# Kernel optimization log

Hardware: AMD Instinct MI355X
Metric: run time of the kernel (lower is better)

The kernel has to match this reference:

```python
import jax, jax.numpy as jnp
import numpy as np
import math

T = 1024      # num tokens
D = 1024      # hidden_size
H = 16        # attention heads
KV = 4        # kv heads
DH = 64       # head_dim
E = 8         # routed experts
K = 2         # top-k
F = 512       # moe_intermediate_size
FS = 2048     # shared_expert_intermediate_size
L = 2         # layers
V = 4096      # codec vocab
THETA = 1e6
EPS = 1e-6


def rms(x, w):
    return x * jax.lax.rsqrt(jnp.mean(x * x, -1, keepdims=True) + EPS) * w


def rope(x, pos):
    # x: [T, h, DH], rotate-half (non-interleaved) rotary
    half = DH // 2
    inv = 1.0 / (THETA ** (jnp.arange(half, dtype=jnp.float32) / half))
    ang = pos.astype(jnp.float32)[:, None] * inv          # [T, half]
    cos = jnp.concatenate([jnp.cos(ang)] * 2, -1)[:, None, :]
    sin = jnp.concatenate([jnp.sin(ang)] * 2, -1)[:, None, :]
    rot = jnp.concatenate([-x[..., half:], x[..., :half]], -1)
    return x * cos + rot * sin


def setup_inputs() -> dict:
    key = jax.random.key(0)
    ks = jax.random.split(key, 20)
    s = 0.02
    n = lambda k, shp: jax.random.normal(k, shp, dtype=jnp.float32) * s
    return {
        "input_ids": jax.random.randint(ks[0], (T,), 0, V),
        "positions": jnp.arange(T),
        "emb": n(ks[1], (V, D)),
        "ln1": jnp.ones((L, D), jnp.float32),
        "wq": n(ks[2], (L, D, H * DH)),
        "wk": n(ks[3], (L, D, KV * DH)),
        "wv": n(ks[4], (L, D, KV * DH)),
        "wo": n(ks[5], (L, H * DH, D)),
        "qn": jnp.ones((L, DH), jnp.float32),
        "kn": jnp.ones((L, DH), jnp.float32),
        "ln2": jnp.ones((L, D), jnp.float32),
        "router_w": n(ks[6], (L, D, E)),
        "egu": n(ks[7], (L, E, D, 2 * F)),
        "edn": n(ks[8], (L, E, F, D)),
        "sgu": n(ks[9], (L, D, 2 * FS)),
        "sdn": n(ks[10], (L, FS, D)),
        "sg_gate": n(ks[11], (L, D)),
        "final_ln": jnp.ones((D,), jnp.float32),
    }


def forward(input_ids, positions, emb, ln1, wq, wk, wv, wo, qn, kn, ln2,
            router_w, egu, edn, sgu, sdn, sg_gate, final_ln):
    h = emb[input_ids]                          # [T, D]
    res = jnp.zeros_like(h)
    causal = jnp.tril(jnp.ones((T, T), bool))
    scale = 1.0 / math.sqrt(DH)
    for i in range(L):
        # --- attention (pre-norm, fused add-residual semantics) ---
        res = h + res
        hn = rms(res, ln1[i])
        q = rms((hn @ wq[i]).reshape(T, H, DH), qn[i])
        k = rms((hn @ wk[i]).reshape(T, KV, DH), kn[i])
        v = (hn @ wv[i]).reshape(T, KV, DH)
        q, k = rope(q, positions), rope(k, positions)
        k = jnp.repeat(k, H // KV, axis=1)      # GQA expand
        v = jnp.repeat(v, H // KV, axis=1)
        att = jnp.einsum('qhd,khd->hqk', q, k) * scale
        att = jnp.where(causal[None], att, -jnp.inf)
        att = jax.nn.softmax(att, axis=-1)
        o = jnp.einsum('hqk,khd->qhd', att, v).reshape(T, H * DH) @ wo[i]
        # --- MoE MLP with shared expert ---
        res = o + res
        hn = rms(res, ln2[i])
        # shared expert: SiluAndMul + down, gated by sigmoid scalar
        gu = hn @ sgu[i]
        shared = (jax.nn.silu(gu[:, :FS]) * gu[:, FS:]) @ sdn[i]
        shared = shared * jax.nn.sigmoid(hn @ sg_gate[i])[:, None]
        # routed experts: softmax router, top-k, renormalize
        probs = jax.nn.softmax(hn @ router_w[i], axis=-1)      # [T, E]
        w, idx = jax.lax.top_k(probs, K)
        w = w / jnp.sum(w, -1, keepdims=True)
        comb = jnp.zeros((T, E), hn.dtype).at[jnp.arange(T)[:, None], idx].add(w)
        g = jnp.einsum('td,edf->tef', hn, egu[i])              # [T, E, 2F]
        he = jax.nn.silu(g[..., :F]) * g[..., F:]              # [T, E, F]
        routed = jnp.einsum('tef,efd,te->td', he, edn[i], comb)
        h = routed + shared
    res = h + res
    return rms(res, final_ln)


def reference(input_ids, positions, emb, ln1, wq, wk, wv, wo, qn, kn, ln2,
              router_w, egu, edn, sgu, sdn, sg_gate, final_ln):
    return forward(input_ids, positions, emb, ln1, wq, wk, wv, wo, qn, kn, ln2,
                   router_w, egu, edn, sgu, sdn, sg_gate, final_ln)
```

## Files before the change

kernel.cpp:

```cpp
#include <hip/hip_runtime.h>
#include <hip/hip_bf16.h>

#define T_ 1024
#define D_ 1024
#define H_ 16
#define KV_ 4
#define DH_ 64
#define E_ 8
#define TOPK_ 2
#define F_ 512
#define FS_ 2048
#define L_ 2

typedef unsigned int uint32;
typedef __attribute__((ext_vector_type(8))) short short8;
typedef __attribute__((ext_vector_type(4))) short short4v;
typedef __attribute__((ext_vector_type(4))) float f32x4;

__device__ __forceinline__ short f2bf(float f){
  uint32 u = __float_as_uint(f);
  return (short)((u + 0x7fffu + ((u >> 16) & 1u)) >> 16);
}
__device__ __forceinline__ float bf2f(short s){
  return __uint_as_float(((uint32)(unsigned short)s) << 16);
}

__device__ __forceinline__ void split8(const float* src, short8& h8, short8& l8){
  #pragma unroll
  for (int j = 0; j < 8; j++){
    short hi = f2bf(src[j]);
    h8[j] = hi;
    l8[j] = f2bf(src[j] - bf2f(hi));
  }
}

__global__ void k_embed(const int* __restrict__ ids, const float* __restrict__ emb,
                        float* __restrict__ h, float* __restrict__ res){
  int idx = blockIdx.x * 256 + threadIdx.x;
  int t = idx >> 10, d = idx & 1023;
  h[idx] = emb[(size_t)ids[t] * D_ + d];
  res[idx] = 0.f;
}

__global__ void k_zero_i32(int* __restrict__ p, int n){
  int i = blockIdx.x * 64 + threadIdx.x;
  if (i < n) p[i] = 0;
}

__global__ __launch_bounds__(256)
void k_fused_rms(float* __restrict__ res, const float* __restrict__ h,
                 const float* __restrict__ w, float* __restrict__ out){
  int t = blockIdx.x, tid = threadIdx.x;
  float* rr = res + (size_t)t * D_;
  const float* hr = h + (size_t)t * D_;
  float ss = 0.f;
  float vloc[4];
  #pragma unroll
  for (int u = 0; u < 4; u++){
    int d = tid + u * 256;
    float v = rr[d] + hr[d];
    vloc[u] = v;
    ss += v * v;
  }
  #pragma unroll
  for (int o = 32; o; o >>= 1) ss += __shfl_xor(ss, o);
  __shared__ float red[4];
  if ((tid & 63) == 0) red[tid >> 6] = ss;
  __syncthreads();
  float r = rsqrtf((red[0] + red[1] + red[2] + red[3]) * (1.f / D_) + 1e-6f);
  float* orow = out + (size_t)t * D_;
  #pragma unroll
  for (int u = 0; u < 4; u++){
    int d = tid + u * 256;
    rr[d] = vloc[u];
    orow[d] = vloc[u] * r * w[d];
  }
}

__global__ __launch_bounds__(256)
void k_fused_rms2(float* __restrict__ res, const float* __restrict__ h0,
                  const float* __restrict__ h1,
                  const float* __restrict__ w, float* __restrict__ out){
  int t = blockIdx.x, tid = threadIdx.x;
  float* rr = res + (size_t)t * D_;
  const float* h0r = h0 + (size_t)t * D_;
  const float* h1r = h1 + (size_t)t * D_;
  float ss = 0.f;
  float vloc[4];
  #pragma unroll
  for (int u = 0; u < 4; u++){
    int d = tid + u * 256;
    float v = rr[d] + h0r[d] + h1r[d];
    vloc[u] = v;
    ss += v * v;
  }
  #pragma unroll
  for (int o = 32; o; o >>= 1) ss += __shfl_xor(ss, o);
  __shared__ float red[4];
  if ((tid & 63) == 0) red[tid >> 6] = ss;
  __syncthreads();
  float r = rsqrtf((red[0] + red[1] + red[2] + red[3]) * (1.f / D_) + 1e-6f);
  float* orow = out + (size_t)t * D_;
  #pragma unroll
  for (int u = 0; u < 4; u++){
    int d = tid + u * 256;
    rr[d] = vloc[u];
    orow[d] = vloc[u] * r * w[d];
  }
}

__global__ __launch_bounds__(64)
void k_qknorm_rope(float* __restrict__ buf, const float* __restrict__ nw,
                   const int* __restrict__ pos, int nheads){
  int row = blockIdx.x;
  int t = row / nheads;
  int lane = threadIdx.x;
  int base = row * DH_ + lane;
  float x = buf[base];
  float ss = x * x;
  #pragma unroll
  for (int o = 32; o; o >>= 1) ss += __shfl_xor(ss, o);
  float r = rsqrtf(ss * (1.f / DH_) + 1e-6f);
  float xn = x * r * nw[lane];
  int j = lane & 31;
  float inv = powf(1.0e6f, -(float)j * (1.f / 32.f));
  float ang = (float)pos[t] * inv;
  float s, c;
  sincosf(ang, &s, &c);
  float p = __shfl_xor(xn, 32);
  float rot = (lane < 32) ? -p : p;
  buf[base] = xn * c + rot * s;
}

__global__ __launch_bounds__(256)
void k_fattn(const float* __restrict__ q, const float* __restrict__ k,
             const float* __restrict__ v, float* __restrict__ out){
  const int h = blockIdx.x, qt = blockIdx.y;
  const int kvh = h >> 2;
  const int tid = threadIdx.x;
  const int w = tid >> 6, lane = tid & 63, l16 = lane & 15, lq = lane >> 4;

  __shared__ __align__(16) short Kh[64][72], Kl[64][72];
  __shared__ __align__(16) short Vth[64][72], Vtl[64][72];
  __shared__ __align__(16) short Ph[64][72], Pl[64][72];

  short8 qh[2], ql[2];
  {
    const float* qp = q + ((size_t)(qt * 64 + w * 16 + l16) * H_ + h) * DH_;
    #pragma unroll
    for (int s = 0; s < 2; s++){
      float a8[8];
      *(float4*)&a8[0] = *(const float4*)(qp + lq * 8 + 32 * s);
      *(float4*)&a8[4] = *(const float4*)(qp + lq * 8 + 32 * s + 4);
      split8(a8, qh[s], ql[s]);
    }
  }

  float m_i[4], l_i[4];
  f32x4 acc[4];
  #pragma unroll
  for (int i = 0; i < 4; i++){ m_i[i] = -1e30f; l_i[i] = 0.f; acc[i] = (f32x4){0.f,0.f,0.f,0.f}; }

  const int kc = tid >> 2, kd = (tid & 3) * 16;
  const int vc0 = (tid & 15) * 4, vd0 = (tid >> 4) * 4;
  float kr[16], vr[16];

  {
    const float* kp = k + ((size_t)(0 + kc) * KV_ + kvh) * DH_ + kd;
    #pragma unroll
    for (int u = 0; u < 16; u += 4) *(float4*)&kr[u] = *(const float4*)(kp + u);
    #pragma unroll
    for (int cc = 0; cc < 4; cc++){
      const float* vp = v + ((size_t)(0 + vc0 + cc) * KV_ + kvh) * DH_ + vd0;
      *(float4*)&vr[cc * 4] = *(const float4*)vp;
    }
  }

  for (int kt = 0; kt <= qt; kt++){
    __syncthreads();
    {
      short8 h8, l8;
      split8(&kr[0], h8, l8);
      *(short8*)&Kh[kc][kd] = h8;     *(short8*)&Kl[kc][kd] = l8;
      split8(&kr[8], h8, l8);
      *(short8*)&Kh[kc][kd + 8] = h8; *(short8*)&Kl[kc][kd + 8] = l8;
      #pragma unroll
      for (int dd = 0; dd < 4; dd++){
        short4v hv, lv;
        #pragma unroll
        for (int cc = 0; cc < 4; cc++){
          float f = vr[cc * 4 + dd];
          short hb = f2bf(f);
          hv[cc] = hb;
          lv[cc] = f2bf(f - bf2f(hb));
        }
        *(short4v*)&Vth[vd0 + dd][vc0] = hv;
        *(short4v*)&Vtl[vd0 + dd][vc0] = lv;
      }
    }
    __syncthreads();
    if (kt < qt){
      const float* kp = k + ((size_t)((kt + 1) * 64 + kc) * KV_ + kvh) * DH_ + kd;
      #pragma unroll
      for (int u = 0; u < 16; u += 4) *(float4*)&kr[u] = *(const float4*)(kp + u);
      #pragma unroll
      for (int cc = 0; cc < 4; cc++){
        const float* vp = v + ((size_t)((kt + 1) * 64 + vc0 + cc) * KV_ + kvh) * DH_ + vd0;
        *(float4*)&vr[cc * 4] = *(const float4*)vp;
      }
    }

    f32x4 sa[4];
    #pragma unroll
    for (int ct = 0; ct < 4; ct++) sa[ct] = (f32x4){0.f,0.f,0.f,0.f};
    #pragma unroll
    for (int s = 0; s < 2; s++){
      #pragma unroll
      for (int ct = 0; ct < 4; ct++){
        short8 kh8 = *(const short8*)&Kh[ct * 16 + l16][lq * 8 + 32 * s];
        short8 kl8 = *(const short8*)&Kl[ct * 16 + l16][lq * 8 + 32 * s];
        sa[ct] = __builtin_amdgcn_mfma_f32_16x16x32_bf16(qh[s], kh8, sa[ct], 0, 0, 0);
        sa[ct] = __builtin_amdgcn_mfma_f32_16x16x32_bf16(qh[s], kl8, sa[ct], 0, 0, 0);
        sa[ct] = __builtin_amdgcn_mfma_f32_16x16x32_bf16(ql[s], kh8, sa[ct], 0, 0, 0);
      }
    }

    const bool diag = (kt == qt);
    #pragma unroll
    for (int ct = 0; ct < 4; ct++)
      #pragma unroll
      for (int i = 0; i < 4; i++){
        float sv = sa[ct][i] * 0.125f;
        if (diag && (ct * 16 + l16 > w * 16 + lq * 4 + i)) sv = -1e30f;
        sa[ct][i] = sv;
      }

    #pragma unroll
    for (int i = 0; i < 4; i++){
      float mx = fmaxf(fmaxf(sa[0][i], sa[1][i]), fmaxf(sa[2][i], sa[3][i]));
      #pragma unroll
      for (int o = 8; o; o >>= 1) mx = fmaxf(mx, __shfl_xor(mx, o));
      float mn = fmaxf(m_i[i], mx);
      float al = __expf(m_i[i] - mn);
      float ls = 0.f;
      #pragma unroll
      for (int ct = 0; ct < 4; ct++){
        float pv = __expf(sa[ct][i] - mn);
        sa[ct][i] = pv;
        ls += pv;
      }
      #pragma unroll
      for (int o = 8; o; o >>= 1) ls += __shfl_xor(ls, o);
      l_i[i] = l_i[i] * al + ls;
      m_i[i] = mn;
      #pragma unroll
      for (int dt = 0; dt < 4; dt++) acc[dt][i] *= al;
    }

    {
      int pr = w * 16 + lq * 4;
      #pragma unroll
      for (int i = 0; i < 4; i++)
        #pragma unroll
        for (int ct = 0; ct < 4; ct++){
          float pv = sa[ct][i];
          short hb = f2bf(pv);
          Ph[pr + i][ct * 16 + l16] = hb;
          Pl[pr + i][ct * 16 + l16] = f2bf(pv - bf2f(hb));
        }
    }
    __syncthreads();

    #pragma unroll
    for (int s = 0; s < 2; s++){
      short8 pah = *(const short8*)&Ph[w * 16 + l16][lq * 8 + 32 * s];
      short8 pal = *(const short8*)&Pl[w * 16 + l16][lq * 8 + 32 * s];
      #pragma unroll
      for (int dt = 0; dt < 4; dt++){
        short8 vh8 = *(const short8*)&Vth[dt * 16 + l16][lq * 8 + 32 * s];
        short8 vl8 = *(const short8*)&Vtl[dt * 16 + l16][lq * 8 + 32 * s];
        acc[dt] = __builtin_amdgcn_mfma_f32_16x16x32_bf16(pah, vh8, acc[dt], 0, 0, 0);
        acc[dt] = __builtin_amdgcn_mfma_f32_16x16x32_bf16(pah, vl8, acc[dt], 0, 0, 0);
        acc[dt] = __builtin_amdgcn_mfma_f32_16x16x32_bf16(pal, vh8, acc[dt], 0, 0, 0);
      }
    }
  }

  int orow = qt * 64 + w * 16 + lq * 4;
  #pragma unroll
  for (int i = 0; i < 4; i++){
    float inv = 1.f / l_i[i];
    #pragma unroll
    for (int dt = 0; dt < 4; dt++)
      out[(size_t)(orow + i) * (H_ * DH_) + h * DH_ + dt * 16 + l16] = acc[dt][i] * inv;
  }
}

#define GEMM_LDS  __shared__ __align__(16) short Ah[64][40], Al[64][40], Bh[64][40], Bl[64][40]

#define GEMM_BODY(APTR, KFULL, KBASE, KH, BPTR, N_, MROW_OK)                                  \
  f32x4 acc[4] = {};                                                                          \
  {                                                                                           \
    int tid = threadIdx.x;                                                                    \
    int w_ = tid >> 6, lane = tid & 63, l16 = lane & 15, lq = lane >> 4;                      \
    int sm = tid & 63, sk = (tid >> 6) * 8;                                                   \
    (void)w_; (void)l16; (void)lq;                                                            \
    const float* Arow = (APTR) + (size_t)(KBASE) + sk;                                        \
    const float* Bcol = (BPTR) + (size_t)((KBASE) + sk) * (N_) + col0 + sm;                   \
    float a_reg[8], b_reg[8];                                                                 \
    if (MROW_OK){                                                                             \
      *(float4*)&a_reg[0] = *(const float4*)(Arow);                                           \
      *(float4*)&a_reg[4] = *(const float4*)(Arow + 4);                                       \
    } else {                                                                                  \
      _Pragma("unroll") for (int j = 0; j < 8; j++) a_reg[j] = 0.f;                           \
    }                                                                                         \
    _Pragma("unroll") for (int j = 0; j < 8; j++) b_reg[j] = Bcol[(size_t)j * (N_)];          \
    int nc = (KH) >> 5;                                                                       \
    for (int c = 0; c < nc; c++){                                                             \
      short8 h8, l8;                                                                          \
      split8(a_reg, h8, l8);                                                                  \
      *(short8*)&Ah[sm][sk] = h8;                                                             \
      *(short8*)&Al[sm][sk] = l8;                                                             \
      split8(b_reg, h8, l8);                                                                  \
      *(short8*)&Bh[sm][sk] = h8;                                                             \
      *(short8*)&Bl[sm][sk] = l8;                                                             \
      __syncthreads();                                                                        \
      if (c + 1 < nc){                                                                        \
        const float* An = Arow + (c + 1) * 32;                                                \
        if (MROW_OK){                                                                         \
          *(float4*)&a_reg[0] = *(const float4*)(An);                                         \
          *(float4*)&a_reg[4] = *(const float4*)(An + 4);                                     \
        }                                                                                     \
        const float* Bn = Bcol + (size_t)(c + 1) * 32 * (N_);                                 \
        _Pragma("unroll") for (int j = 0; j < 8; j++) b_reg[j] = Bn[(size_t)j * (N_)];        \
      }                                                                                       \
      short8 ah = *(const short8*)&Ah[w_ * 16 + l16][lq * 8];                                 \
      short8 al = *(const short8*)&Al[w_ * 16 + l16][lq * 8];                                 \
      _Pragma("unroll")                                                                       \
      for (int nt = 0; nt < 4; nt++){                                                         \
        short8 bh = *(const short8*)&Bh[nt * 16 + l16][lq * 8];                               \
        short8 bl = *(const short8*)&Bl[nt * 16 + l16][lq * 8];                               \
        acc[nt] = __builtin_amdgcn_mfma_f32_16x16x32_bf16(ah, bh, acc[nt], 0, 0, 0);          \
        acc[nt] = __builtin_amdgcn_mfma_f32_16x16x32_bf16(ah, bl, acc[nt], 0, 0, 0);          \
        acc[nt] = __builtin_amdgcn_mfma_f32_16x16x32_bf16(al, bh, acc[nt], 0, 0, 0);          \
      }                                                                                       \
      __syncthreads();                                                                        \
    }                                                                                         \
  }

__global__ __launch_bounds__(256)
void k_mgemm(const float* __restrict__ A, const float* __restrict__ B,
             float* __restrict__ C, int M, int N, int K){
  GEMM_LDS;
  int row0 = blockIdx.y * 64, col0 = blockIdx.x * 64;
  int sm = threadIdx.x & 63;
  bool aok = (row0 + sm) < M;
  const float* Abase = A + (size_t)(row0 + sm) * K;
  GEMM_BODY(Abase, K, 0, K, B, N, aok);
  int w = threadIdx.x >> 6, lane = threadIdx.x & 63, l16 = lane & 15, lq = lane >> 4;
  #pragma unroll
  for (int nt = 0; nt < 4; nt++)
    #pragma unroll
    for (int i = 0; i < 4; i++){
      int r = row0 + w * 16 + lq * 4 + i;
      if (r < M) C[(size_t)r * N + col0 + nt * 16 + l16] = acc[nt][i];
    }
}

__global__ __launch_bounds__(256)
void k_mgemm_ks2(const float* __restrict__ A, const float* __restrict__ B,
                 float* __restrict__ C0, float* __restrict__ C1,
                 int M, int N, int K){
  GEMM_LDS;
  int row0 = blockIdx.y * 64, col0 = blockIdx.x * 64;
  int z = blockIdx.z, KH = K >> 1;
  int sm = threadIdx.x & 63;
  bool aok = (row0 + sm) < M;
  const float* Abase = A + (size_t)(row0 + sm) * K;
  GEMM_BODY(Abase, K, z * KH, KH, B, N, aok);
  float* C = z ? C1 : C0;
  int w = threadIdx.x >> 6, lane = threadIdx.x & 63, l16 = lane & 15, lq = lane >> 4;
  #pragma unroll
  for (int nt = 0; nt < 4; nt++)
    #pragma unroll
    for (int i = 0; i < 4; i++){
      int r = row0 + w * 16 + lq * 4 + i;
      if (r < M) C[(size_t)r * N + col0 + nt * 16 + l16] = acc[nt][i];
    }
}

__global__ __launch_bounds__(256)
void k_mgemm_qkv(const float* __restrict__ hn, const float* __restrict__ wq_l,
                 const float* __restrict__ wk_l, const float* __restrict__ wv_l,
                 float* __restrict__ qlin, float* __restrict__ kbuf,
                 float* __restrict__ vbuf){
  GEMM_LDS;
  int cb = blockIdx.x;
  const float* B; float* C; int N; int col0;
  if (cb < 16){ B = wq_l; C = qlin; N = H_ * DH_; col0 = cb * 64; }
  else if (cb < 20){ B = wk_l; C = kbuf; N = KV_ * DH_; col0 = (cb - 16) * 64; }
  else { B = wv_l; C = vbuf; N = KV_ * DH_; col0 = (cb - 20) * 64; }
  int row0 = blockIdx.y * 64;
  int sm = threadIdx.x & 63;
  const float* Abase = hn + (size_t)(row0 + sm) * D_;
  GEMM_BODY(Abase, D_, 0, D_, B, N, true);
  int w = threadIdx.x >> 6, lane = threadIdx.x & 63, l16 = lane & 15, lq = lane >> 4;
  #pragma unroll
  for (int nt = 0; nt < 4; nt++)
    #pragma unroll
    for (int i = 0; i < 4; i++){
      int r = row0 + w * 16 + lq * 4 + i;
      C[(size_t)r * N + col0 + nt * 16 + l16] = acc[nt][i];
    }
}

__global__ __launch_bounds__(256)
void k_mgemm_up(const float* __restrict__ hn, const float* __restrict__ egu_l,
                float* __restrict__ G0, float* __restrict__ G1,
                const int* __restrict__ counts, const int* __restrict__ offsets,
                const int* __restrict__ rowtok){
  const int z = blockIdx.z;
  const int e = z >> 1, s = z & 1;
  const int me = counts[e];
  const int row0 = blockIdx.y * 64;
  if (row0 >= me) return;
  const int off = offsets[e];
  const float* B = egu_l + (size_t)e * D_ * (2 * F_);
  const int N = 2 * F_, KH = D_ >> 1;
  GEMM_LDS;
  int col0 = blockIdx.x * 64;
  int sm = threadIdx.x & 63;
  bool aok = (row0 + sm) < me;
  int tok = aok ? rowtok[off + row0 + sm] : 0;
  const float* Abase = hn + (size_t)tok * D_;
  GEMM_BODY(Abase, D_, s * KH, KH, B, N, aok);
  float* G = s ? G1 : G0;
  int w = threadIdx.x >> 6, lane = threadIdx.x & 63, l16 = lane & 15, lq = lane >> 4;
  #pragma unroll
  for (int nt = 0; nt < 4; nt++)
    #pragma unroll
    for (int i = 0; i < 4; i++){
      int r = row0 + w * 16 + lq * 4 + i;
      if (r < me) G[(size_t)(off + r) * N + col0 + nt * 16 + l16] = acc[nt][i];
    }
}

__global__ __launch_bounds__(256)
void k_mgemm_dn(const float* __restrict__ he, const float* __restrict__ edn_l,
                float* __restrict__ routed, const int* __restrict__ counts,
                const int* __restrict__ offsets, const int* __restrict__ rowtok,
                const float* __restrict__ roww){
  const int z = blockIdx.z;
  const int e = z >> 1, s = z & 1;
  const int me = counts[e];
  const int row0 = blockIdx.y * 64;
  if (row0 >= me) return;
  const int off = offsets[e];
  const float* B = edn_l + (size_t)e * F_ * D_;
  const int N = D_, KH = F_ >> 1;
  GEMM_LDS;
  int col0 = blockIdx.x * 64;
  int sm = threadIdx.x & 63;
  bool aok = (row0 + sm) < me;
  const float* Abase = he + (size_t)(off + row0 + (aok ? sm : 0)) * F_;
  GEMM_BODY(Abase, F_, s * KH, KH, B, N, aok);
  int w = threadIdx.x >> 6, lane = threadIdx.x & 63, l16 = lane & 15, lq = lane >> 4;
  #pragma unroll
  for (int i = 0; i < 4; i++){
    int r = row0 + w * 16 + lq * 4 + i;
    if (r < me){
      int tok = rowtok[off + r];
      float wgt = roww[off + r];
      float* cp = routed + (size_t)tok * D_ + col0;
      #pragma unroll
      for (int nt = 0; nt < 4; nt++)
        atomicAdd(&cp[nt * 16 + l16], wgt * acc[nt][i]);
    }
  }
}

__global__ void k_silumul(const float* __restrict__ g, float* __restrict__ out,
                          int width, int half){
  int idx = blockIdx.x * 256 + threadIdx.x;
  int r = idx / half, f = idx - r * half;
  float a = g[(size_t)r * width + f];
  float b = g[(size_t)r * width + half + f];
  out[idx] = a * b / (1.f + __expf(-a));
}

__global__ void k_silumul2(const float* __restrict__ g0, const float* __restrict__ g1,
                           float* __restrict__ out, int width, int half){
  int idx = blockIdx.x * 256 + threadIdx.x;
  int r = idx / half, f = idx - r * half;
  size_t ia = (size_t)r * width + f, ib = (size_t)r * width + half + f;
  float a = g0[ia] + g1[ia];
  float b = g0[ib] + g1[ib];
  out[idx] = a * b / (1.f + __expf(-a));
}

__global__ __launch_bounds__(256)
void k_gate(const float* __restrict__ hn, const float* __restrict__ sg,
            float* __restrict__ gate){
  int t = blockIdx.x, tid = threadIdx.x;
  const float* xr = hn + (size_t)t * D_;
  float s = 0.f;
  for (int d = tid; d < D_; d += 256) s += xr[d] * sg[d];
  #pragma unroll
  for (int o = 32; o; o >>= 1) s += __shfl_xor(s, o);
  __shared__ float red[4];
  if ((tid & 63) == 0) red[tid >> 6] = s;
  __syncthreads();
  if (tid == 0){
    float tot = red[0] + red[1] + red[2] + red[3];
    gate[t] = 1.f / (1.f + __expf(-tot));
  }
}

__global__ __launch_bounds__(64)
void k_router(const float* __restrict__ hn, const float* __restrict__ rw,
              int* __restrict__ counts, int* __restrict__ top_e,
              float* __restrict__ top_w){
  int t = blockIdx.x;
  int lane = threadIdx.x;
  int e = lane & 7, c = lane >> 3;
  const float* xr = hn + (size_t)t * D_;
  float s = 0.f;
  for (int d = c * 128; d < c * 128 + 128; d++) s += xr[d] * rw[d * E_ + e];
  s += __shfl_down(s, 32);
  s += __shfl_down(s, 16);
  s += __shfl_down(s, 8);
  float v[8];
  #pragma unroll
  for (int qq = 0; qq < 8; qq++) v[qq] = __shfl(s, qq);
  if (lane == 0){
    float mx = v[0];
    #pragma unroll
    for (int qq = 1; qq < 8; qq++) mx = fmaxf(mx, v[qq]);
    float p[8];
    #pragma unroll
    for (int qq = 0; qq < 8; qq++) p[qq] = __expf(v[qq] - mx);
    int i0 = 0;
    #pragma unroll
    for (int qq = 1; qq < 8; qq++) if (p[qq] > p[i0]) i0 = qq;
    int i1 = (i0 == 0) ? 1 : 0;
    #pragma unroll
    for (int qq = 0; qq < 8; qq++) if (qq != i0 && p[qq] > p[i1]) i1 = qq;
    float w0 = p[i0], w1 = p[i1];
    float inv = 1.f / (w0 + w1);
    top_e[t * 2 + 0] = i0; top_w[t * 2 + 0] = w0 * inv;
    top_e[t * 2 + 1] = i1; top_w[t * 2 + 1] = w1 * inv;
    atomicAdd(&counts[i0], 1);
    atomicAdd(&counts[i1], 1);
  }
}

__global__ void k_prefix(const int* __restrict__ counts, int* __restrict__ offsets,
                         int* __restrict__ cursor){
  if (threadIdx.x == 0 && blockIdx.x == 0){
    int acc = 0;
    for (int e = 0; e < E_; e++){ offsets[e] = acc; cursor[e] = acc; acc += counts[e]; }
  }
}

__global__ void k_assign(const int* __restrict__ top_e, const float* __restrict__ top_w,
                         int* __restrict__ cursor, int* __restrict__ rowtok,
                         float* __restrict__ roww){
  int i = blockIdx.x * 256 + threadIdx.x;
  if (i >= T_ * TOPK_) return;
  int e = top_e[i];
  int slot = atomicAdd(&cursor[e], 1);
  rowtok[slot] = i >> 1;
  roww[slot] = top_w[i];
}

__global__ void k_prefill2(float* __restrict__ h, const float* __restrict__ p0,
                           const float* __restrict__ p1, const float* __restrict__ gate){
  int idx = blockIdx.x * 256 + threadIdx.x;
  h[idx] = (p0[idx] + p1[idx]) * gate[idx >> 10];
}

__global__ __launch_bounds__(256)
void k_final_rms(const float* __restrict__ resv, const float* __restrict__ hv,
                 const float* __restrict__ w, float* __restrict__ out){
  int t = blockIdx.x, tid = threadIdx.x;
  const float* xr = resv + (size_t)t * D_;
  const float* hr = hv + (size_t)t * D_;
  float ss = 0.f;
  for (int d = tid; d < D_; d += 256){ float v = xr[d] + hr[d]; ss += v * v; }
  #pragma unroll
  for (int o = 32; o; o >>= 1) ss += __shfl_xor(ss, o);
  __shared__ float red[4];
  if ((tid & 63) == 0) red[tid >> 6] = ss;
  __syncthreads();
  float r = rsqrtf((red[0] + red[1] + red[2] + red[3]) * (1.f / D_) + 1e-6f);
  float* orow = out + (size_t)t * D_;
  for (int d = tid; d < D_; d += 256) orow[d] = (xr[d] + hr[d]) * r * w[d];
}

extern "C" void kernel_launch(void* const* d_in, const int* in_sizes, int n_in,
                              void* d_out, int out_size, void* d_ws, size_t ws_size,
                              hipStream_t stream){
  (void)in_sizes; (void)n_in; (void)out_size; (void)ws_size;
  const int* ids = (const int*)d_in[0];
  const int* pos = (const int*)d_in[1];
  const float* emb = (const float*)d_in[2];
  const float* ln1 = (const float*)d_in[3];
  const float* wq  = (const float*)d_in[4];
  const float* wk  = (const float*)d_in[5];
  const float* wv  = (const float*)d_in[6];
  const float* wo  = (const float*)d_in[7];
  const float* qn  = (const float*)d_in[8];
  const float* kn  = (const float*)d_in[9];
  const float* ln2 = (const float*)d_in[10];
  const float* rw  = (const float*)d_in[11];
  const float* egu = (const float*)d_in[12];
  const float* edn = (const float*)d_in[13];
  const float* sgu = (const float*)d_in[14];
  const float* sdn = (const float*)d_in[15];
  const float* sg  = (const float*)d_in[16];
  const float* fln = (const float*)d_in[17];

  float* ws = (float*)d_ws;
  const size_t MB = (size_t)1 << 20;
  float* res    = ws;
  float* h      = ws + 1 * MB;
  float* hn     = ws + 2 * MB;
  float* qlin   = ws + 3 * MB;
  float* kbuf   = ws + 4 * MB;
  float* vbuf   = kbuf + T_ * KV_ * DH_;
  float* attnb  = ws + 5 * MB;
  float* gu     = ws + 6 * MB;
  float* sact   = ws + 10 * MB;
  float* ps0    = ws + 12 * MB;
  float* G0     = ws + 13 * MB;
  float* he     = ws + 15 * MB;
  float* ps1    = ws + 16 * MB;
  float* gate   = ws + 17 * MB;
  float* roww   = gate + 4096;
  float* top_w  = roww + 4096;
  int* counts   = (int*)(top_w + 4096);
  int* offsets  = counts + 8;
  int* cursor   = offsets + 8;
  int* top_e    = cursor + 8;
  int* rowtok   = top_e + 2048;
  float* G1     = ws + 3 * MB;
  float* pw0    = ws + 3 * MB;
  float* pw1    = ws + 4 * MB;

  const int NTD = T_ * D_ / 256;

  k_embed<<<NTD, 256, 0, stream>>>(ids, emb, h, res);

  for (int i = 0; i < L_; i++){
    k_fused_rms<<<T_, 256, 0, stream>>>(res, h, ln1 + (size_t)i * D_, hn);
    k_mgemm_qkv<<<dim3(24, 16), 256, 0, stream>>>(hn,
        wq + (size_t)i * D_ * (H_ * DH_), wk + (size_t)i * D_ * (KV_ * DH_),
        wv + (size_t)i * D_ * (KV_ * DH_), qlin, kbuf, vbuf);
    k_qknorm_rope<<<T_ * H_, 64, 0, stream>>>(qlin, qn + (size_t)i * DH_, pos, H_);
    k_qknorm_rope<<<T_ * KV_, 64, 0, stream>>>(kbuf, kn + (size_t)i * DH_, pos, KV_);
    k_fattn<<<dim3(H_, T_ / 64), 256, 0, stream>>>(qlin, kbuf, vbuf, attnb);
    k_mgemm_ks2<<<dim3(16, 16, 2), 256, 0, stream>>>(attnb, wo + (size_t)i * (H_ * DH_) * D_,
                                                     pw0, pw1, T_, D_, H_ * DH_);
    k_fused_rms2<<<T_, 256, 0, stream>>>(res, pw0, pw1, ln2 + (size_t)i * D_, hn);
    k_mgemm<<<dim3(64, 16), 256, 0, stream>>>(hn, sgu + (size_t)i * D_ * (2 * FS_), gu, T_, 2 * FS_, D_);
    k_silumul<<<T_ * FS_ / 256, 256, 0, stream>>>(gu, sact, 2 * FS_, FS_);
    k_mgemm_ks2<<<dim3(16, 16, 2), 256, 0, stream>>>(sact, sdn + (size_t)i * FS_ * D_,
                                                     ps0, ps1, T_, D_, FS_);
    k_gate<<<T_, 256, 0, stream>>>(hn, sg + (size_t)i * D_, gate);
    k_zero_i32<<<1, 64, 0, stream>>>(counts, 8);
    k_router<<<T_, 64, 0, stream>>>(hn, rw + (size_t)i * D_ * E_, counts, top_e, top_w);
    k_prefix<<<1, 1, 0, stream>>>(counts, offsets, cursor);
    k_assign<<<8, 256, 0, stream>>>(top_e, top_w, cursor, rowtok, roww);
    k_mgemm_up<<<dim3(16, 32, 16), 256, 0, stream>>>(hn, egu + (size_t)i * E_ * D_ * (2 * F_),
                                                     G0, G1, counts, offsets, rowtok);
    k_silumul2<<<T_ * TOPK_ * F_ / 256, 256, 0, stream>>>(G0, G1, he, 2 * F_, F_);
    k_prefill2<<<NTD, 256, 0, stream>>>(h, ps0, ps1, gate);
    k_mgemm_dn<<<dim3(16, 32, 16), 256, 0, stream>>>(he, edn + (size_t)i * E_ * F_ * D_,
                                                     h, counts, offsets, rowtok, roww);
  }

  k_final_rms<<<T_, 256, 0, stream>>>(res, h, fln, (float*)d_out);
}
```

Baseline: 907.4 us.

## Pre-split weights and activations into transposed bf16 hi/lo buffers for GEMMs

```diff
diff --git a/kernel.cpp b/kernel.cpp
--- a/kernel.cpp
+++ b/kernel.cpp
@@ -13,6 +13,7 @@
 #define L_ 2
 
 typedef unsigned int uint32;
+typedef unsigned short u16;
 typedef __attribute__((ext_vector_type(8))) short short8;
 typedef __attribute__((ext_vector_type(4))) short short4v;
 typedef __attribute__((ext_vector_type(4))) float f32x4;
@@ -48,8 +49,31 @@
 }
 
 __global__ __launch_bounds__(256)
+void k_wconvT2(const float* __restrict__ in, u16* __restrict__ outh,
+               u16* __restrict__ outl, int K, int N){
+  __shared__ float tile[64][65];
+  const int kb = blockIdx.y * 64, nb = blockIdx.x * 64;
+  const size_t slab = (size_t)blockIdx.z * K * N;
+  in += slab; outh += slab; outl += slab;
+  int tx = threadIdx.x & 63, ty0 = threadIdx.x >> 6;
+  #pragma unroll 4
+  for (int uy = ty0; uy < 64; uy += 4)
+    tile[uy][tx] = in[(size_t)(kb + uy) * N + nb + tx];
+  __syncthreads();
+  #pragma unroll 4
+  for (int uy = ty0; uy < 64; uy += 4){
+    float x = tile[tx][uy];
+    short hb = f2bf(x);
+    size_t o = (size_t)(nb + uy) * K + kb + tx;
+    outh[o] = (u16)hb;
+    outl[o] = (u16)f2bf(x - bf2f(hb));
+  }
+}
+
+__global__ __launch_bounds__(256)
 void k_fused_rms(float* __restrict__ res, const float* __restrict__ h,
-                 const float* __restrict__ w, float* __restrict__ out){
+                 const float* __restrict__ w, float* __restrict__ out,
+                 u16* __restrict__ oh, u16* __restrict__ ol){
   int t = blockIdx.x, tid = threadIdx.x;
   float* rr = res + (size_t)t * D_;
   const float* hr = h + (size_t)t * D_;
@@ -73,14 +97,18 @@
   for (int u = 0; u < 4; u++){
     int d = tid + u * 256;
     rr[d] = vloc[u];
-    orow[d] = vloc[u] * r * w[d];
+    float o = vloc[u] * r * w[d];
+    orow[d] = o;
+    short hb = f2bf(o);
+    oh[(size_t)t * D_ + d] = (u16)hb;
+    ol[(size_t)t * D_ + d] = (u16)f2bf(o - bf2f(hb));
   }
 }
 
 __global__ __launch_bounds__(256)
 void k_fused_rms2(float* __restrict__ res, const float* __restrict__ h0,
-                  const float* __restrict__ h1,
-                  const float* __restrict__ w, float* __restrict__ out){
+                  const float* __restrict__ h1, const float* __restrict__ w,
+                  float* __restrict__ out, u16* __restrict__ oh, u16* __restrict__ ol){
   int t = blockIdx.x, tid = threadIdx.x;
   float* rr = res + (size_t)t * D_;
   const float* h0r = h0 + (size_t)t * D_;
@@ -105,7 +133,11 @@
   for (int u = 0; u < 4; u++){
     int d = tid + u * 256;
     rr[d] = vloc[u];
-    orow[d] = vloc[u] * r * w[d];
+    float o = vloc[u] * r * w[d];
+    orow[d] = o;
+    short hb = f2bf(o);
+    oh[(size_t)t * D_ + d] = (u16)hb;
+    ol[(size_t)t * D_ + d] = (u16)f2bf(o - bf2f(hb));
   }
 }
 
@@ -134,7 +166,8 @@
 
 __global__ __launch_bounds__(256)
 void k_fattn(const float* __restrict__ q, const float* __restrict__ k,
-             const float* __restrict__ v, float* __restrict__ out){
+             const float* __restrict__ v, u16* __restrict__ outh,
+             u16* __restrict__ outl){
   const int h = blockIdx.x, qt = blockIdx.y;
   const int kvh = h >> 2;
   const int tid = threadIdx.x;
@@ -291,72 +324,74 @@
   for (int i = 0; i < 4; i++){
     float inv = 1.f / l_i[i];
     #pragma unroll
-    for (int dt = 0; dt < 4; dt++)
-      out[(size_t)(orow + i) * (H_ * DH_) + h * DH_ + dt * 16 + l16] = acc[dt][i] * inv;
-  }
-}
-
-#define GEMM_LDS  __shared__ __align__(16) short Ah[64][40], Al[64][40], Bh[64][40], Bl[64][40]
-
-#define GEMM_BODY(APTR, KFULL, KBASE, KH, BPTR, N_, MROW_OK)                                  \
+    for (int dt = 0; dt < 4; dt++){
+      size_t oidx = (size_t)(orow + i) * (H_ * DH_) + h * DH_ + dt * 16 + l16;
+      float o = acc[dt][i] * inv;
+      short hb = f2bf(o);
+      outh[oidx] = (u16)hb;
+      outl[oidx] = (u16)f2bf(o - bf2f(hb));
+    }
+  }
+}
+
+#define GEMM_LDS4  __shared__ __align__(16) short Ah[64][40], Al[64][40], Bh[64][40], Bl[64][40]
+
+#define GEMM_BODY4(ARH, ARL, BRH, BRL, KBASE, KH, AOK)                                        \
   f32x4 acc[4] = {};                                                                          \
   {                                                                                           \
     int tid = threadIdx.x;                                                                    \
-    int w_ = tid >> 6, lane = tid & 63, l16 = lane & 15, lq = lane >> 4;                      \
-    int sm = tid & 63, sk = (tid >> 6) * 8;                                                   \
-    (void)w_; (void)l16; (void)lq;                                                            \
-    const float* Arow = (APTR) + (size_t)(KBASE) + sk;                                        \
-    const float* Bcol = (BPTR) + (size_t)((KBASE) + sk) * (N_) + col0 + sm;                   \
-    float a_reg[8], b_reg[8];                                                                 \
-    if (MROW_OK){                                                                             \
-      *(float4*)&a_reg[0] = *(const float4*)(Arow);                                           \
-      *(float4*)&a_reg[4] = *(const float4*)(Arow + 4);                                       \
-    } else {                                                                                  \
-      _Pragma("unroll") for (int j = 0; j < 8; j++) a_reg[j] = 0.f;                           \
-    }                                                                                         \
-    _Pragma("unroll") for (int j = 0; j < 8; j++) b_reg[j] = Bcol[(size_t)j * (N_)];          \
+    int w_ = tid >> 6, lane_ = tid & 63, l16_ = lane_ & 15, lq_ = lane_ >> 4;                 \
+    int sm_ = tid & 63, sk_ = (tid >> 6) * 8;                                                 \
+    const u16* pAh = (ARH) + (KBASE) + sk_;                                                   \
+    const u16* pAl = (ARL) + (KBASE) + sk_;                                                   \
+    const u16* pBh = (BRH) + (KBASE) + sk_;                                                   \
+    const u16* pBl = (BRL) + (KBASE) + sk_;                                                   \
+    short8 a_h = {}, a_l = {}, b_h, b_l;                                                      \
+    if (AOK){ a_h = *(const short8*)pAh; a_l = *(const short8*)pAl; }                         \
+    b_h = *(const short8*)pBh;                                                                \
+    b_l = *(const short8*)pBl;                                                                \
     int nc = (KH) >> 5;                                                                       \
     for (int c = 0; c < nc; c++){                                                             \
-      short8 h8, l8;                                                                          \
-      split8(a_reg, h8, l8);                                                                  \
-      *(short8*)&Ah[sm][sk] = h8;                                                             \
-      *(short8*)&Al[sm][sk] = l8;                                                             \
-      split8(b_reg, h8, l8);                                                                  \
-      *(short8*)&Bh[sm][sk] = h8;                                                             \
-      *(short8*)&Bl[sm][sk] = l8;                                                             \
+      *(short8*)&Ah[sm_][sk_] = a_h;                                                          \
+      *(short8*)&Al[sm_][sk_] = a_l;                                                          \
+      *(short8*)&Bh[sm_][sk_] = b_h;                                                          \
+      *(short8*)&Bl[sm_][sk_] = b_l;                                                          \
       __syncthreads();                                                                        \
       if (c + 1 < nc){                                                                        \
-        const float* An = Arow + (c + 1) * 32;                                                \
-        if (MROW_OK){                                                                         \
-          *(float4*)&a_reg[0] = *(const float4*)(An);                                         \
-          *(float4*)&a_reg[4] = *(const float4*)(An + 4);                                     \
+        if (AOK){                                                                             \
+          a_h = *(const short8*)(pAh + (c + 1) * 32);                                         \
+          a_l = *(const short8*)(pAl + (c + 1) * 32);                                         \
         }                                                                                     \
-        const float* Bn = Bcol + (size_t)(c + 1) * 32 * (N_);                                 \
-        _Pragma("unroll") for (int j = 0; j < 8; j++) b_reg[j] = Bn[(size_t)j * (N_)];        \
+        b_h = *(const short8*)(pBh + (c + 1) * 32);                                           \
+        b_l = *(const short8*)(pBl + (c + 1) * 32);                                           \
       }                                                                                       \
-      short8 ah = *(const short8*)&Ah[w_ * 16 + l16][lq * 8];                                 \
-      short8 al = *(const short8*)&Al[w_ * 16 + l16][lq * 8];                                 \
+      short8 fa = *(const short8*)&Ah[w_ * 16 + l16_][lq_ * 8];                               \
+      short8 fl = *(const short8*)&Al[w_ * 16 + l16_][lq_ * 8];                               \
       _Pragma("unroll")                                                                       \
       for (int nt = 0; nt < 4; nt++){                                                         \
-        short8 bh = *(const short8*)&Bh[nt * 16 + l16][lq * 8];                               \
-        short8 bl = *(const short8*)&Bl[nt * 16 + l16][lq * 8];                               \
-        acc[nt] = __builtin_amdgcn_mfma_f32_16x16x32_bf16(ah, bh, acc[nt], 0, 0, 0);          \
-        acc[nt] = __builtin_amdgcn_mfma_f32_16x16x32_bf16(ah, bl, acc[nt], 0, 0, 0);          \
-        acc[nt] = __builtin_amdgcn_mfma_f32_16x16x32_bf16(al, bh, acc[nt], 0, 0, 0);          \
+        short8 fbh = *(const short8*)&Bh[nt * 16 + l16_][lq_ * 8];                            \
+        short8 fbl = *(const short8*)&Bl[nt * 16 + l16_][lq_ * 8];                            \
+        acc[nt] = __builtin_amdgcn_mfma_f32_16x16x32_bf16(fa, fbh, acc[nt], 0, 0, 0);         \
+        acc[nt] = __builtin_amdgcn_mfma_f32_16x16x32_bf16(fa, fbl, acc[nt], 0, 0, 0);         \
+        acc[nt] = __builtin_amdgcn_mfma_f32_16x16x32_bf16(fl, fbh, acc[nt], 0, 0, 0);         \
       }                                                                                       \
       __syncthreads();                                                                        \
     }                                                                                         \
   }
 
 __global__ __launch_bounds__(256)
-void k_mgemm(const float* __restrict__ A, const float* __restrict__ B,
+void k_bgemm(const u16* __restrict__ A_h, const u16* __restrict__ A_l,
+             const u16* __restrict__ Bth, const u16* __restrict__ Btl,
              float* __restrict__ C, int M, int N, int K){
-  GEMM_LDS;
+  GEMM_LDS4;
   int row0 = blockIdx.y * 64, col0 = blockIdx.x * 64;
   int sm = threadIdx.x & 63;
   bool aok = (row0 + sm) < M;
-  const float* Abase = A + (size_t)(row0 + sm) * K;
-  GEMM_BODY(Abase, K, 0, K, B, N, aok);
+  const u16* Ar = A_h + (size_t)(row0 + sm) * K;
+  const u16* Lr = A_l + (size_t)(row0 + sm) * K;
+  const u16* Bch = Bth + (size_t)(col0 + sm) * K;
+  const u16* Bcl = Btl + (size_t)(col0 + sm) * K;
+  GEMM_BODY4(Ar, Lr, Bch, Bcl, 0, K, aok);
   int w = threadIdx.x >> 6, lane = threadIdx.x & 63, l16 = lane & 15, lq = lane >> 4;
   #pragma unroll
   for (int nt = 0; nt < 4; nt++)
@@ -368,16 +403,20 @@
 }
 
 __global__ __launch_bounds__(256)
-void k_mgemm_ks2(const float* __restrict__ A, const float* __restrict__ B,
+void k_bgemm_ks2(const u16* __restrict__ A_h, const u16* __restrict__ A_l,
+                 const u16* __restrict__ Bth, const u16* __restrict__ Btl,
                  float* __restrict__ C0, float* __restrict__ C1,
                  int M, int N, int K){
-  GEMM_LDS;
+  GEMM_LDS4;
   int row0 = blockIdx.y * 64, col0 = blockIdx.x * 64;
   int z = blockIdx.z, KH = K >> 1;
   int sm = threadIdx.x & 63;
   bool aok = (row0 + sm) < M;
-  const float* Abase = A + (size_t)(row0 + sm) * K;
-  GEMM_BODY(Abase, K, z * KH, KH, B, N, aok);
+  const u16* Ar = A_h + (size_t)(row0 + sm) * K;
+  const u16* Lr = A_l + (size_t)(row0 + sm) * K;
+  const u16* Bch = Bth + (size_t)(col0 + sm) * K;
+  const u16* Bcl = Btl + (size_t)(col0 + sm) * K;
+  GEMM_BODY4(Ar, Lr, Bch, Bcl, z * KH, KH, aok);
   float* C = z ? C1 : C0;
   int w = threadIdx.x >> 6, lane = threadIdx.x & 63, l16 = lane & 15, lq = lane >> 4;
   #pragma unroll
@@ -390,20 +429,25 @@
 }
 
 __global__ __launch_bounds__(256)
-void k_mgemm_qkv(const float* __restrict__ hn, const float* __restrict__ wq_l,
-                 const float* __restrict__ wk_l, const float* __restrict__ wv_l,
+void k_bgemm_qkv(const u16* __restrict__ hn_h, const u16* __restrict__ hn_l,
+                 const u16* __restrict__ wqh, const u16* __restrict__ wql,
+                 const u16* __restrict__ wkh, const u16* __restrict__ wkl,
+                 const u16* __restrict__ wvh, const u16* __restrict__ wvl,
                  float* __restrict__ qlin, float* __restrict__ kbuf,
                  float* __restrict__ vbuf){
-  GEMM_LDS;
+  GEMM_LDS4;
   int cb = blockIdx.x;
-  const float* B; float* C; int N; int col0;
-  if (cb < 16){ B = wq_l; C = qlin; N = H_ * DH_; col0 = cb * 64; }
-  else if (cb < 20){ B = wk_l; C = kbuf; N = KV_ * DH_; col0 = (cb - 16) * 64; }
-  else { B = wv_l; C = vbuf; N = KV_ * DH_; col0 = (cb - 20) * 64; }
+  const u16 *Bth, *Btl; float* C; int N; int col0;
+  if (cb < 16){ Bth = wqh; Btl = wql; C = qlin; N = H_ * DH_; col0 = cb * 64; }
+  else if (cb < 20){ Bth = wkh; Btl = wkl; C = kbuf; N = KV_ * DH_; col0 = (cb - 16) * 64; }
+  else { Bth = wvh; Btl = wvl; C = vbuf; N = KV_ * DH_; col0 = (cb - 20) * 64; }
   int row0 = blockIdx.y * 64;
   int sm = threadIdx.x & 63;
-  const float* Abase = hn + (size_t)(row0 + sm) * D_;
-  GEMM_BODY(Abase, D_, 0, D_, B, N, true);
+  const u16* Ar = hn_h + (size_t)(row0 + sm) * D_;
+  const u16* Lr = hn_l + (size_t)(row0 + sm) * D_;
+  const u16* Bch = Bth + (size_t)(col0 + sm) * D_;
+  const u16* Bcl = Btl + (size_t)(col0 + sm) * D_;
+  GEMM_BODY4(Ar, Lr, Bch, Bcl, 0, D_, true);
   int w = threadIdx.x >> 6, lane = threadIdx.x & 63, l16 = lane & 15, lq = lane >> 4;
   #pragma unroll
   for (int nt = 0; nt < 4; nt++)
@@ -415,7 +459,8 @@
 }
 
 __global__ __launch_bounds__(256)
-void k_mgemm_up(const float* __restrict__ hn, const float* __restrict__ egu_l,
+void k_bgemm_up(const u16* __restrict__ hn_h, const u16* __restrict__ hn_l,
+                const u16* __restrict__ eguh, const u16* __restrict__ egul,
                 float* __restrict__ G0, float* __restrict__ G1,
                 const int* __restrict__ counts, const int* __restrict__ offsets,
                 const int* __restrict__ rowtok){
@@ -425,15 +470,17 @@
   const int row0 = blockIdx.y * 64;
   if (row0 >= me) return;
   const int off = offsets[e];
-  const float* B = egu_l + (size_t)e * D_ * (2 * F_);
   const int N = 2 * F_, KH = D_ >> 1;
-  GEMM_LDS;
+  GEMM_LDS4;
   int col0 = blockIdx.x * 64;
   int sm = threadIdx.x & 63;
   bool aok = (row0 + sm) < me;
   int tok = aok ? rowtok[off + row0 + sm] : 0;
-  const float* Abase = hn + (size_t)tok * D_;
-  GEMM_BODY(Abase, D_, s * KH, KH, B, N, aok);
+  const u16* Ar = hn_h + (size_t)tok * D_;
+  const u16* Lr = hn_l + (size_t)tok * D_;
+  const u16* Bch = eguh + ((size_t)e * (2 * F_) + col0 + sm) * D_;
+  const u16* Bcl = egul + ((size_t)e * (2 * F_) + col0 + sm) * D_;
+  GEMM_BODY4(Ar, Lr, Bch, Bcl, s * KH, KH, aok);
   float* G = s ? G1 : G0;
   int w = threadIdx.x >> 6, lane = threadIdx.x & 63, l16 = lane & 15, lq = lane >> 4;
   #pragma unroll
@@ -446,7 +493,8 @@
 }
 
 __global__ __launch_bounds__(256)
-void k_mgemm_dn(const float* __restrict__ he, const float* __restrict__ edn_l,
+void k_bgemm_dn(const u16* __restrict__ he_h, const u16* __restrict__ he_l,
+                const u16* __restrict__ ednh, const u16* __restrict__ ednl,
                 float* __restrict__ routed, const int* __restrict__ counts,
                 const int* __restrict__ offsets, const int* __restrict__ rowtok,
                 const float* __restrict__ roww){
@@ -456,14 +504,16 @@
   const int row0 = blockIdx.y * 64;
   if (row0 >= me) return;
   const int off = offsets[e];
-  const float* B = edn_l + (size_t)e * F_ * D_;
-  const int N = D_, KH = F_ >> 1;
-  GEMM_LDS;
+  const int KH = F_ >> 1;
+  GEMM_LDS4;
   int col0 = blockIdx.x * 64;
   int sm = threadIdx.x & 63;
   bool aok = (row0 + sm) < me;
-  const float* Abase = he + (size_t)(off + row0 + (aok ? sm : 0)) * F_;
-  GEMM_BODY(Abase, F_, s * KH, KH, B, N, aok);
+  const u16* Ar = he_h + (size_t)(off + row0 + (aok ? sm : 0)) * F_;
+  const u16* Lr = he_l + (size_t)(off + row0 + (aok ? sm : 0)) * F_;
+  const u16* Bch = ednh + ((size_t)e * D_ + col0 + sm) * F_;
+  const u16* Bcl = ednl + ((size_t)e * D_ + col0 + sm) * F_;
+  GEMM_BODY4(Ar, Lr, Bch, Bcl, s * KH, KH, aok);
   int w = threadIdx.x >> 6, lane = threadIdx.x & 63, l16 = lane & 15, lq = lane >> 4;
   #pragma unroll
   for (int i = 0; i < 4; i++){
@@ -479,23 +529,30 @@
   }
 }
 
-__global__ void k_silumul(const float* __restrict__ g, float* __restrict__ out,
-                          int width, int half){
+__global__ void k_silumul(const float* __restrict__ g, u16* __restrict__ oh,
+                          u16* __restrict__ ol, int width, int half){
   int idx = blockIdx.x * 256 + threadIdx.x;
   int r = idx / half, f = idx - r * half;
   float a = g[(size_t)r * width + f];
   float b = g[(size_t)r * width + half + f];
-  out[idx] = a * b / (1.f + __expf(-a));
+  float val = a * b / (1.f + __expf(-a));
+  short hb = f2bf(val);
+  oh[idx] = (u16)hb;
+  ol[idx] = (u16)f2bf(val - bf2f(hb));
 }
 
 __global__ void k_silumul2(const float* __restrict__ g0, const float* __restrict__ g1,
-                           float* __restrict__ out, int width, int half){
+                           u16* __restrict__ oh, u16* __restrict__ ol,
+                           int width, int half){
   int idx = blockIdx.x * 256 + threadIdx.x;
   int r = idx / half, f = idx - r * half;
   size_t ia = (size_t)r * width + f, ib = (size_t)r * width + half + f;
   float a = g0[ia] + g1[ia];
   float b = g0[ib] + g1[ib];
-  out[idx] = a * b / (1.f + __expf(-a));
+  float val = a * b / (1.f + __expf(-a));
+  short hb = f2bf(val);
+  oh[idx] = (u16)hb;
+  ol[idx] = (u16)f2bf(val - bf2f(hb));
 }
 
 __global__ __launch_bounds__(256)
@@ -628,14 +685,19 @@
   float* qlin   = ws + 3 * MB;
   float* kbuf   = ws + 4 * MB;
   float* vbuf   = kbuf + T_ * KV_ * DH_;
-  float* attnb  = ws + 5 * MB;
+  u16* attnb_h  = (u16*)(ws + 5 * MB);
+  u16* attnb_l  = attnb_h + (T_ * H_ * DH_);
   float* gu     = ws + 6 * MB;
-  float* sact   = ws + 10 * MB;
+  u16* sact_h   = (u16*)(ws + 10 * MB);
+  u16* sact_l   = sact_h + (T_ * FS_);
   float* ps0    = ws + 12 * MB;
   float* G0     = ws + 13 * MB;
-  float* he     = ws + 15 * MB;
+  u16* he_h     = (u16*)(ws + 15 * MB);
+  u16* he_l     = he_h + (T_ * TOPK_ * F_);
   float* ps1    = ws + 16 * MB;
-  float* gate   = ws + 17 * MB;
+  u16* hn_h     = (u16*)(ws + 17 * MB);
+  u16* hn_l     = hn_h + (T_ * D_);
+  float* gate   = ws + 18 * MB;
   float* roww   = gate + 4096;
   float* top_w  = roww + 4096;
   int* counts   = (int*)(top_w + 4096);
@@ -643,39 +705,55 @@
   int* cursor   = offsets + 8;
   int* top_e    = cursor + 8;
   int* rowtok   = top_e + 2048;
-  float* G1     = ws + 3 * MB;
-  float* pw0    = ws + 3 * MB;
-  float* pw1    = ws + 4 * MB;
+  u16* W = (u16*)(ws + 18 * MB + (MB >> 2));
+  u16* wq_th = W;                  u16* wq_tl = W + (1u << 20);
+  u16* wk_th = W + (2u << 20);     u16* wk_tl = wk_th + (1u << 18);
+  u16* wv_th = wk_th + (1u << 19); u16* wv_tl = wv_th + (1u << 18);
+  u16* wo_th = W + (3u << 20);     u16* wo_tl = W + (4u << 20);
+  u16* sgu_th = W;                 u16* sgu_tl = W + (4u << 20);
+  u16* sdn_th = W;                 u16* sdn_tl = W + (2u << 20);
+  u16* egu_th = W;                 u16* egu_tl = W + (8u << 20);
+  u16* edn_th = W;                 u16* edn_tl = W + (4u << 20);
+  float* pw0 = ws + 3 * MB;
+  float* pw1 = ws + 4 * MB;
+  float* G1  = ws + 3 * MB;
 
   const int NTD = T_ * D_ / 256;
 
   k_embed<<<NTD, 256, 0, stream>>>(ids, emb, h, res);
 
   for (int i = 0; i < L_; i++){
-    k_fused_rms<<<T_, 256, 0, stream>>>(res, h, ln1 + (size_t)i * D_, hn);
-    k_mgemm_qkv<<<dim3(24, 16), 256, 0, stream>>>(hn,
-        wq + (size_t)i * D_ * (H_ * DH_), wk + (size_t)i * D_ * (KV_ * DH_),
-        wv + (size_t)i * D_ * (KV_ * DH_), qlin, kbuf, vbuf);
+    k_wconvT2<<<dim3(16, 16, 1), 256, 0, stream>>>(wq + (size_t)i * D_ * (H_ * DH_), wq_th, wq_tl, D_, H_ * DH_);
+    k_wconvT2<<<dim3(4, 16, 1), 256, 0, stream>>>(wk + (size_t)i * D_ * (KV_ * DH_), wk_th, wk_tl, D_, KV_ * DH_);
+    k_wconvT2<<<dim3(4, 16, 1), 256, 0, stream>>>(wv + (size_t)i * D_ * (KV_ * DH_), wv_th, wv_tl, D_, KV_ * DH_);
+    k_wconvT2<<<dim3(16, 16, 1), 256, 0, stream>>>(wo + (size_t)i * (H_ * DH_) * D_, wo_th, wo_tl, H_ * DH_, D_);
+    k_fused_rms<<<T_, 256, 0, stream>>>(res, h, ln1 + (size_t)i * D_, hn, hn_h, hn_l);
+    k_bgemm_qkv<<<dim3(24, 16), 256, 0, stream>>>(hn_h, hn_l, wq_th, wq_tl, wk_th, wk_tl,
+                                                  wv_th, wv_tl, qlin, kbuf, vbuf);
     k_qknorm_rope<<<T_ * H_, 64, 0, stream>>>(qlin, qn + (size_t)i * DH_, pos, H_);
     k_qknorm_rope<<<T_ * KV_, 64, 0, stream>>>(kbuf, kn + (size_t)i * DH_, pos, KV_);
-    k_fattn<<<dim3(H_, T_ / 64), 256, 0, stream>>>(qlin, kbuf, vbuf, attnb);
-    k_mgemm_ks2<<<dim3(16, 16, 2), 256, 0, stream>>>(attnb, wo + (size_t)i * (H_ * DH_) * D_,
+    k_fattn<<<dim3(H_, T_ / 64), 256, 0, stream>>>(qlin, kbuf, vbuf, attnb_h, attnb_l);
+    k_bgemm_ks2<<<dim3(16, 16, 2), 256, 0, stream>>>(attnb_h, attnb_l, wo_th, wo_tl,
                                                      pw0, pw1, T_, D_, H_ * DH_);
-    k_fused_rms2<<<T_, 256, 0, stream>>>(res, pw0, pw1, ln2 + (size_t)i * D_, hn);
-    k_mgemm<<<dim3(64, 16), 256, 0, stream>>>(hn, sgu + (size_t)i * D_ * (2 * FS_), gu, T_, 2 * FS_, D_);
-    k_silumul<<<T_ * FS_ / 256, 256, 0, stream>>>(gu, sact, 2 * FS_, FS_);
-    k_mgemm_ks2<<<dim3(16, 16, 2), 256, 0, stream>>>(sact, sdn + (size_t)i * FS_ * D_,
+    k_fused_rms2<<<T_, 256, 0, stream>>>(res, pw0, pw1, ln2 + (size_t)i * D_, hn, hn_h, hn_l);
+    k_wconvT2<<<dim3(64, 16, 1), 256, 0, stream>>>(sgu + (size_t)i * D_ * (2 * FS_), sgu_th, sgu_tl, D_, 2 * FS_);
+    k_bgemm<<<dim3(64, 16), 256, 0, stream>>>(hn_h, hn_l, sgu_th, sgu_tl, gu, T_, 2 * FS_, D_);
+    k_wconvT2<<<dim3(16, 32, 1), 256, 0, stream>>>(sdn + (size_t)i * FS_ * D_, sdn_th, sdn_tl, FS_, D_);
+    k_silumul<<<T_ * FS_ / 256, 256, 0, stream>>>(gu, sact_h, sact_l, 2 * FS_, FS_);
+    k_bgemm_ks2<<<dim3(16, 16, 2), 256, 0, stream>>>(sact_h, sact_l, sdn_th, sdn_tl,
                                                      ps0, ps1, T_, D_, FS_);
     k_gate<<<T_, 256, 0, stream>>>(hn, sg + (size_t)i * D_, gate);
     k_zero_i32<<<1, 64, 0, stream>>>(counts, 8);
     k_router<<<T_, 64, 0, stream>>>(hn, rw + (size_t)i * D_ * E_, counts, top_e, top_w);
     k_prefix<<<1, 1, 0, stream>>>(counts, offsets, cursor);
     k_assign<<<8, 256, 0, stream>>>(top_e, top_w, cursor, rowtok, roww);
-    k_mgemm_up<<<dim3(16, 32, 16), 256, 0, stream>>>(hn, egu + (size_t)i * E_ * D_ * (2 * F_),
+    k_prefill2<<<NTD, 256, 0, stream>>>(h, ps0, ps1, gate);
+    k_wconvT2<<<dim3(16, 16, E_), 256, 0, stream>>>(egu + (size_t)i * E_ * D_ * (2 * F_), egu_th, egu_tl, D_, 2 * F_);
+    k_bgemm_up<<<dim3(16, 32, 16), 256, 0, stream>>>(hn_h, hn_l, egu_th, egu_tl,
                                                      G0, G1, counts, offsets, rowtok);
-    k_silumul2<<<T_ * TOPK_ * F_ / 256, 256, 0, stream>>>(G0, G1, he, 2 * F_, F_);
-    k_prefill2<<<NTD, 256, 0, stream>>>(h, ps0, ps1, gate);
-    k_mgemm_dn<<<dim3(16, 32, 16), 256, 0, stream>>>(he, edn + (size_t)i * E_ * F_ * D_,
+    k_silumul2<<<T_ * TOPK_ * F_ / 256, 256, 0, stream>>>(G0, G1, he_h, he_l, 2 * F_, F_);
+    k_wconvT2<<<dim3(16, 8, E_), 256, 0, stream>>>(edn + (size_t)i * E_ * F_ * D_, edn_th, edn_tl, F_, D_);
+    k_bgemm_dn<<<dim3(16, 32, 16), 256, 0, stream>>>(he_h, he_l, edn_th, edn_tl,
                                                      h, counts, offsets, rowtok, roww);
   }
 
```

New measurement: 1.107 ms. +22.0%, slower.
